# Kernel optimization log

Measured on AMD Instinct MI355X. Metric: run time of the kernel, lower is better.

Reference implementation:

```python
import jax, jax.numpy as jnp
import numpy as np

N_QUBITS = 4
DIM = 16  # 2**N_QUBITS
BATCH = 2_097_152


def _pauli_sign_tables():
    # Wire 0 is the most-significant bit in pennylane default.qubit ordering.
    bits = (np.arange(DIM)[:, None] >> np.arange(N_QUBITS - 1, -1, -1)[None, :]) & 1
    z_signs = (1 - 2 * bits).astype(np.float32)  # [16, 4], <Z_i> signs per basis state
    pairs = [(i, j) for i in range(N_QUBITS) for j in range(i + 1, N_QUBITS)]
    zz_signs = np.stack([z_signs[:, i] * z_signs[:, j] for i, j in pairs], axis=1)  # [16, 6]
    return jnp.asarray(z_signs), jnp.asarray(zz_signs)

Z_SIGNS, ZZ_SIGNS = _pauli_sign_tables()


def setup_inputs() -> dict:
    key = jax.random.key(0)
    ks = jax.random.split(key, 6)
    return {
        "x": jax.random.normal(ks[0], (BATCH, DIM), jnp.float32),
        "u_weights": jax.random.normal(ks[1], (N_QUBITS, 2), jnp.float32),
        "w1": jax.random.normal(ks[2], (16, 10), jnp.float32) * 0.3,
        "b1": jnp.zeros((16,), jnp.float32),
        "w2": jax.random.normal(ks[3], (2, 16), jnp.float32) * 0.25,
        "b2": jnp.zeros((2,), jnp.float32),
    }


def _circuit_features(x, u_weights):
    # StatePrep with normalize=True
    state = x / jnp.linalg.norm(x, axis=1, keepdims=True)
    state = state.astype(jnp.complex64).reshape(-1, 2, 2, 2, 2)  # [B, q0, q1, q2, q3]
    half_th = 0.5 * u_weights[:, 0]
    half_ph = 0.5 * u_weights[:, 1]
    c, s = jnp.cos(half_th), jnp.sin(half_th)
    for q in range(N_QUBITS):
        ry = jnp.stack([jnp.stack([c[q], -s[q]]),
                        jnp.stack([s[q], c[q]])]).astype(jnp.complex64)
        e = jnp.exp(-1j * half_ph[q].astype(jnp.complex64))
        rz = jnp.diag(jnp.stack([e, jnp.conj(e)]))
        u = rz @ ry  # RZ(phi) after RY(theta), single fused 2x2 gate
        state = jnp.moveaxis(state, q + 1, -1)
        state = state @ u.T  # new[a] = sum_b u[a,b] * old[b]
        state = jnp.moveaxis(state, -1, q + 1)
    probs = jnp.abs(state.reshape(-1, DIM)) ** 2  # [B, 16]
    z = probs @ Z_SIGNS    # [B, 4]  <Z_i>
    zz = probs @ ZZ_SIGNS  # [B, 6]  <Z_i Z_j>, i<j
    return jnp.concatenate([z, zz], axis=1)  # [B, 10]


def reference(x, u_weights, w1, b1, w2, b2):
    feats = _circuit_features(x, u_weights)
    h = jax.nn.relu(feats @ w1.T + b1)
    return h @ w2.T + b2  # [B, 2]
```

## Files before the change

kernel.cpp:

```cpp
#include <hip/hip_runtime.h>
#include <math.h>


#define PAD 20

__global__ __launch_bounds__(256) void qc_fused(
    const float* __restrict__ x, const float* __restrict__ uw,
    const float* __restrict__ w1, const float* __restrict__ b1,
    const float* __restrict__ w2, const float* __restrict__ b2,
    float* __restrict__ out, int batch)
{
    __shared__ float sX[256 * PAD];
    __shared__ float sW1t[160];
    __shared__ float sB1[16];
    __shared__ float sW2[32];
    __shared__ float sB2[2];
    __shared__ float sCS[8];

    const int t = threadIdx.x;

    if (t < 4) {
        float th = 0.5f * uw[2 * t];
        sCS[t]     = cosf(th);
        sCS[4 + t] = sinf(th);
    }
    if (t < 160) sW1t[t] = w1[(t & 15) * 10 + (t >> 4)];
    if (t < 16)  sB1[t] = b1[t];
    if (t < 32)  sW2[t] = w2[t];
    if (t < 2)   sB2[t] = b2[t];

    const float4* xv4 = (const float4*)x;
    const long nv4 = (long)batch * 4;
    const long base4 = (long)blockIdx.x * 1024;
#pragma unroll
    for (int r2 = 0; r2 < 4; ++r2) {
        int f = t + 256 * r2;
        long g = base4 + f;
        float4 v = (g < nv4) ? xv4[g] : make_float4(0.f, 0.f, 0.f, 0.f);
        ((float4*)(sX + (f >> 2) * PAD))[f & 3] = v;
    }
    __syncthreads();

    const float* myx = sX + t * PAD;
    float y[16];
#pragma unroll
    for (int i = 0; i < 4; ++i) {
        float4 v = ((const float4*)myx)[i];
        y[4 * i + 0] = v.x; y[4 * i + 1] = v.y;
        y[4 * i + 2] = v.z; y[4 * i + 3] = v.w;
    }

    float ss = 0.f;
#pragma unroll
    for (int i = 0; i < 16; ++i) ss = fmaf(y[i], y[i], ss);
    const float rn = 1.0f / ss;

#pragma unroll
    for (int q = 0; q < 4; ++q) {
        const float cq = sCS[q], sq = sCS[4 + q];
        const int st = 8 >> q;
#pragma unroll
        for (int i = 0; i < 16; ++i) {
            if ((i & st) == 0) {
                float a = y[i], b = y[i + st];
                y[i]      = fmaf(cq, a, -sq * b);
                y[i + st] = fmaf(sq, a,  cq * b);
            }
        }
    }

    float p[16];
#pragma unroll
    for (int i = 0; i < 16; ++i) p[i] = y[i] * y[i];
#pragma unroll
    for (int st = 1; st < 16; st <<= 1) {
#pragma unroll
        for (int i = 0; i < 16; ++i) {
            if ((i & st) == 0) {
                float a = p[i], b = p[i + st];
                p[i]      = a + b;
                p[i + st] = a - b;
            }
        }
    }

    constexpr int bmap[10] = {8, 4, 2, 1, 12, 10, 9, 6, 5, 3};

    float tacc[16];
#pragma unroll
    for (int j = 0; j < 16; ++j) tacc[j] = 0.f;
#pragma unroll
    for (int f = 0; f < 10; ++f) {
        const float ff = p[bmap[f]];
        const float* col = sW1t + f * 16;
#pragma unroll
        for (int j = 0; j < 16; ++j) tacc[j] = fmaf(col[j], ff, tacc[j]);
    }

    float o0 = sB2[0], o1 = sB2[1];
#pragma unroll
    for (int j = 0; j < 16; ++j) {
        float h = fmaf(tacc[j], rn, sB1[j]);
        h = fmaxf(h, 0.f);
        o0 = fmaf(sW2[j],      h, o0);
        o1 = fmaf(sW2[16 + j], h, o1);
    }

    const long sidx = (long)blockIdx.x * 256 + t;
    if (sidx < batch) ((float2*)out)[sidx] = make_float2(o0, o1);
}

extern "C" void kernel_launch(void* const* d_in, const int* in_sizes, int n_in,
                              void* d_out, int out_size, void* d_ws, size_t ws_size,
                              hipStream_t stream) {
    const float* x  = (const float*)d_in[0];
    const float* uw = (const float*)d_in[1];
    const float* w1 = (const float*)d_in[2];
    const float* b1 = (const float*)d_in[3];
    const float* w2 = (const float*)d_in[4];
    const float* b2 = (const float*)d_in[5];
    float* out = (float*)d_out;

    int batch = in_sizes[0] / 16;
    int blocks = (batch + 255) / 256;
    hipLaunchKernelGGL(qc_fused, dim3(blocks), dim3(256), 0, stream,
                       x, uw, w1, b1, w2, b2, out, batch);
}
```

Before: 208.8 us.

## Load rows directly to registers, two samples per thread, weights from global

Drops the shared-memory staging of x. Each thread now loads its 64-byte rows straight from global as float4s and processes two samples, which doubles ILP and halves the block count. Weights and biases are read directly from global (likely scalar/constant loads) instead of shared. The norm is taken from the Hadamard DC term p[0], which is invariant under the rotations. Uncoalesced per-thread strided float4 loads may reduce memory efficiency compared with the staged, coalesced path, and register pressure rises.

Result: no change. 208.3 us (-0.2%).

```diff
diff --git a/kernel.cpp b/kernel.cpp
--- a/kernel.cpp
+++ b/kernel.cpp
@@ -1,113 +1,118 @@
 #include <hip/hip_runtime.h>
 #include <math.h>
 
-
-#define PAD 20
 
 __global__ __launch_bounds__(256) void qc_fused(
     const float* __restrict__ x, const float* __restrict__ uw,
     const float* __restrict__ w1, const float* __restrict__ b1,
     const float* __restrict__ w2, const float* __restrict__ b2,
-    float* __restrict__ out, int batch)
+    float* __restrict__ out, long batch)
 {
-    __shared__ float sX[256 * PAD];
-    __shared__ float sW1t[160];
-    __shared__ float sB1[16];
-    __shared__ float sW2[32];
-    __shared__ float sB2[2];
     __shared__ float sCS[8];
-
     const int t = threadIdx.x;
-
-    if (t < 4) {
-        float th = 0.5f * uw[2 * t];
-        sCS[t]     = cosf(th);
-        sCS[4 + t] = sinf(th);
-    }
-    if (t < 160) sW1t[t] = w1[(t & 15) * 10 + (t >> 4)];
-    if (t < 16)  sB1[t] = b1[t];
-    if (t < 32)  sW2[t] = w2[t];
-    if (t < 2)   sB2[t] = b2[t];
-
-    const float4* xv4 = (const float4*)x;
-    const long nv4 = (long)batch * 4;
-    const long base4 = (long)blockIdx.x * 1024;
-#pragma unroll
-    for (int r2 = 0; r2 < 4; ++r2) {
-        int f = t + 256 * r2;
-        long g = base4 + f;
-        float4 v = (g < nv4) ? xv4[g] : make_float4(0.f, 0.f, 0.f, 0.f);
-        ((float4*)(sX + (f >> 2) * PAD))[f & 3] = v;
+    if (t < 8) {
+        int q = t & 3;
+        float th = 0.5f * uw[2 * q];
+        sCS[t] = (t < 4) ? cosf(th) : sinf(th);
     }
     __syncthreads();
 
-    const float* myx = sX + t * PAD;
-    float y[16];
+    const long base = (long)blockIdx.x * 512 + t;
+    const float4* __restrict__ xv = (const float4*)x;
+
+    float y[2][16];
 #pragma unroll
-    for (int i = 0; i < 4; ++i) {
-        float4 v = ((const float4*)myx)[i];
-        y[4 * i + 0] = v.x; y[4 * i + 1] = v.y;
-        y[4 * i + 2] = v.z; y[4 * i + 3] = v.w;
+    for (int u = 0; u < 2; ++u) {
+        const long s = base + 256 * u;
+        if (s < batch) {
+#pragma unroll
+            for (int i = 0; i < 4; ++i) {
+                float4 v = xv[s * 4 + i];
+                y[u][4 * i + 0] = v.x; y[u][4 * i + 1] = v.y;
+                y[u][4 * i + 2] = v.z; y[u][4 * i + 3] = v.w;
+            }
+        } else {
+#pragma unroll
+            for (int i = 0; i < 16; ++i) y[u][i] = (i == 0) ? 1.f : 0.f;
+        }
     }
 
-    float ss = 0.f;
+    float cs[4], sn[4];
 #pragma unroll
-    for (int i = 0; i < 16; ++i) ss = fmaf(y[i], y[i], ss);
-    const float rn = 1.0f / ss;
+    for (int q = 0; q < 4; ++q) { cs[q] = sCS[q]; sn[q] = sCS[4 + q]; }
 
 #pragma unroll
     for (int q = 0; q < 4; ++q) {
-        const float cq = sCS[q], sq = sCS[4 + q];
         const int st = 8 >> q;
 #pragma unroll
         for (int i = 0; i < 16; ++i) {
             if ((i & st) == 0) {
-                float a = y[i], b = y[i + st];
-                y[i]      = fmaf(cq, a, -sq * b);
-                y[i + st] = fmaf(sq, a,  cq * b);
+#pragma unroll
+                for (int u = 0; u < 2; ++u) {
+                    float a = y[u][i], b = y[u][i + st];
+                    y[u][i]      = fmaf(cs[q], a, -sn[q] * b);
+                    y[u][i + st] = fmaf(sn[q], a,  cs[q] * b);
+                }
             }
         }
     }
 
-    float p[16];
+    float p[2][16];
 #pragma unroll
-    for (int i = 0; i < 16; ++i) p[i] = y[i] * y[i];
+    for (int u = 0; u < 2; ++u)
+#pragma unroll
+        for (int i = 0; i < 16; ++i) p[u][i] = y[u][i] * y[u][i];
 #pragma unroll
     for (int st = 1; st < 16; st <<= 1) {
 #pragma unroll
         for (int i = 0; i < 16; ++i) {
             if ((i & st) == 0) {
-                float a = p[i], b = p[i + st];
-                p[i]      = a + b;
-                p[i + st] = a - b;
+#pragma unroll
+                for (int u = 0; u < 2; ++u) {
+                    float a = p[u][i], b = p[u][i + st];
+                    p[u][i]      = a + b;
+                    p[u][i + st] = a - b;
+                }
             }
         }
     }
 
+    const float rn0 = 1.0f / p[0][0];
+    const float rn1 = 1.0f / p[1][0];
+
     constexpr int bmap[10] = {8, 4, 2, 1, 12, 10, 9, 6, 5, 3};
 
-    float tacc[16];
+    float tacc[2][16];
 #pragma unroll
-    for (int j = 0; j < 16; ++j) tacc[j] = 0.f;
+    for (int j = 0; j < 16; ++j) { tacc[0][j] = 0.f; tacc[1][j] = 0.f; }
 #pragma unroll
     for (int f = 0; f < 10; ++f) {
-        const float ff = p[bmap[f]];
-        const float* col = sW1t + f * 16;
+        const float pa = p[0][bmap[f]];
+        const float pb = p[1][bmap[f]];
 #pragma unroll
-        for (int j = 0; j < 16; ++j) tacc[j] = fmaf(col[j], ff, tacc[j]);
+        for (int j = 0; j < 16; ++j) {
+            const float wv = w1[j * 10 + f];
+            tacc[0][j] = fmaf(wv, pa, tacc[0][j]);
+            tacc[1][j] = fmaf(wv, pb, tacc[1][j]);
+        }
     }
 
-    float o0 = sB2[0], o1 = sB2[1];
+    float o00 = b2[0], o01 = b2[1];
+    float o10 = b2[0], o11 = b2[1];
 #pragma unroll
     for (int j = 0; j < 16; ++j) {
-        float h = fmaf(tacc[j], rn, sB1[j]);
-        h = fmaxf(h, 0.f);
-        o0 = fmaf(sW2[j],      h, o0);
-        o1 = fmaf(sW2[16 + j], h, o1);
+        const float bb  = b1[j];
+        const float w20 = w2[j];
+        const float w21 = w2[16 + j];
+        float ha = fmaxf(fmaf(tacc[0][j], rn0, bb), 0.f);
+        float hb = fmaxf(fmaf(tacc[1][j], rn1, bb), 0.f);
+        o00 = fmaf(w20, ha, o00);  o01 = fmaf(w21, ha, o01);
+        o10 = fmaf(w20, hb, o10);  o11 = fmaf(w21, hb, o11);
     }
 
-    const long sidx = (long)blockIdx.x * 256 + t;
-    if (sidx < batch) ((float2*)out)[sidx] = make_float2(o0, o1);
+    float2* __restrict__ o2 = (float2*)out;
+    if (base < batch)       o2[base]       = make_float2(o00, o01);
+    if (base + 256 < batch) o2[base + 256] = make_float2(o10, o11);
 }
 
 extern "C" void kernel_launch(void* const* d_in, const int* in_sizes, int n_in,
@@ -121,8 +126,8 @@
     const float* b2 = (const float*)d_in[5];
     float* out = (float*)d_out;
 
-    int batch = in_sizes[0] / 16;
-    int blocks = (batch + 255) / 256;
-    hipLaunchKernelGGL(qc_fused, dim3(blocks), dim3(256), 0, stream,
+    long batch = (long)(in_sizes[0] / 16);
+    long blocks = (batch + 511) / 512;
+    hipLaunchKernelGGL(qc_fused, dim3((unsigned)blocks), dim3(256), 0, stream,
                        x, uw, w1, b1, w2, b2, out, batch);
 }
```
